# Optimization experiments

Measured on AMD Instinct MI355X. Metric: run time of the kernel, lower is better.

The kernel has to match this reference:

```python
import jax, jax.numpy as jnp
import numpy as np

C = 512
GROUPS = 32
EPS = 1e-6


def group_norm(x, w, b):
    # x: [B, C, H, W]
    B, Cc, H, W = x.shape
    xg = x.reshape(B, GROUPS, Cc // GROUPS, H, W)
    mean = xg.mean(axis=(2, 3, 4), keepdims=True)
    var = xg.var(axis=(2, 3, 4), keepdims=True)
    xn = (xg - mean) * jax.lax.rsqrt(var + EPS)
    xn = xn.reshape(B, Cc, H, W)
    return xn * w[None, :, None, None] + b[None, :, None, None]


def conv1x1(x, w, b):
    # 1x1 conv == per-pixel linear: w [Cout, Cin], x [B, Cin, H, W]
    return jnp.einsum('oc,bchw->bohw', w, x) + b[None, :, None, None]


def setup_inputs() -> dict:
    key = jax.random.key(0)
    ks = jax.random.split(key, 11)
    B, H, W = 4, 64, 64
    s = 1.0 / np.sqrt(C)
    return {
        'x': jax.random.normal(ks[0], (B, C, H, W), dtype=jnp.float32),
        'gn_w': jnp.ones((C,), dtype=jnp.float32),
        'gn_b': jnp.zeros((C,), dtype=jnp.float32),
        'wq': jax.random.normal(ks[1], (C, C), dtype=jnp.float32) * s,
        'bq': jnp.zeros((C,), dtype=jnp.float32),
        'wk': jax.random.normal(ks[2], (C, C), dtype=jnp.float32) * s,
        'bk': jnp.zeros((C,), dtype=jnp.float32),
        'wv': jax.random.normal(ks[3], (C, C), dtype=jnp.float32) * s,
        'bv': jnp.zeros((C,), dtype=jnp.float32),
        'wo': jax.random.normal(ks[4], (C, C), dtype=jnp.float32) * s,
        'bo': jnp.zeros((C,), dtype=jnp.float32),
    }


def reference(x, gn_w, gn_b, wq, bq, wk, bk, wv, bv, wo, bo):
    B, Cc, H, W = x.shape
    scale = Cc ** (-0.5)
    xn = group_norm(x, gn_w, gn_b)
    q = conv1x1(xn, wq, bq).reshape(B, Cc, H * W)
    k = conv1x1(xn, wk, bk).reshape(B, Cc, H * W)
    v = conv1x1(xn, wv, bv).reshape(B, Cc, H * W)
    attn = jax.nn.softmax(jnp.einsum('bci,bcj->bij', q, k) * scale, axis=2)
    out = jnp.einsum('bij,bcj->bci', attn, v).reshape(B, Cc, H, W)
    out = conv1x1(out, wo, bo)
    return x + out
```

## Files before the change

kernel.cpp:

```cpp
#include <hip/hip_runtime.h>

#define NB 4
#define CC 512
#define NSP 4096
#define NGRP 32

using bf16x8 = __attribute__((ext_vector_type(8))) __bf16;
using f32x4  = __attribute__((ext_vector_type(4))) float;

__device__ __forceinline__ unsigned short f2bf(float f) {
  union { float f; unsigned int u; } v; v.f = f;
  unsigned int r = v.u + 0x7fffu + ((v.u >> 16) & 1u);
  return (unsigned short)(r >> 16);
}
__device__ __forceinline__ float bf2f(unsigned short h) {
  union { unsigned int u; float f; } v; v.u = ((unsigned int)h) << 16;
  return v.f;
}

__global__ __launch_bounds__(256) void cvt_w_kernel(const float* __restrict__ wq,
    const float* __restrict__ wk, const float* __restrict__ wv,
    const float* __restrict__ wo, const float* __restrict__ bq,
    const float* __restrict__ bk, unsigned short* __restrict__ wqk,
    unsigned short* __restrict__ wv_bf, unsigned short* __restrict__ wo_bf,
    float* __restrict__ bias_qk, float scale) {
  int i = blockIdx.x * 256 + threadIdx.x;
  wqk[i]          = f2bf(wq[i] * scale);
  wqk[i + 262144] = f2bf(wk[i]);
  wv_bf[i] = f2bf(wv[i]);
  wo_bf[i] = f2bf(wo[i]);
  if (i < 512)        bias_qk[i] = bq[i] * scale;
  else if (i < 1024)  bias_qk[i] = bk[i - 512];
}

__global__ __launch_bounds__(256) void gn_stats_kernel(const float* __restrict__ x,
                                                       float* __restrict__ stats) {
  const int b = blockIdx.x >> 5, g = blockIdx.x & 31;
  const float4* p = reinterpret_cast<const float4*>(x + ((size_t)b * CC + g * 16) * NSP);
  float s = 0.f, ss = 0.f;
  for (int i = threadIdx.x; i < 16384; i += 256) {
    float4 v = p[i];
    s  += v.x + v.y + v.z + v.w;
    ss += v.x * v.x + v.y * v.y + v.z * v.z + v.w * v.w;
  }
  __shared__ float rs[4], rss[4];
  #pragma unroll
  for (int o = 32; o >= 1; o >>= 1) { s += __shfl_down(s, o); ss += __shfl_down(ss, o); }
  if ((threadIdx.x & 63) == 0) { rs[threadIdx.x >> 6] = s; rss[threadIdx.x >> 6] = ss; }
  __syncthreads();
  if (threadIdx.x == 0) {
    s = rs[0] + rs[1] + rs[2] + rs[3];
    ss = rss[0] + rss[1] + rss[2] + rss[3];
    float mean = s * (1.f / 65536.f);
    float var = ss * (1.f / 65536.f) - mean * mean;
    stats[blockIdx.x * 2 + 0] = mean;
    stats[blockIdx.x * 2 + 1] = rsqrtf(var + 1e-6f);
  }
}

__global__ __launch_bounds__(256) void gn_apply_kernel(const float* __restrict__ x,
    const float* __restrict__ stats, const float* __restrict__ gw,
    const float* __restrict__ gb, unsigned short* __restrict__ xnT) {
  const int b = blockIdx.z, c0 = blockIdx.y * 32, n0 = blockIdx.x * 32;
  __shared__ unsigned short tile[32][33];
  const int tx = threadIdx.x & 31, ty = threadIdx.x >> 5;
  #pragma unroll
  for (int r = 0; r < 4; ++r) {
    const int cl = ty + r * 8;
    const int c = c0 + cl;
    const int g = c >> 4;
    const float mean = stats[(b * 32 + g) * 2];
    const float rstd = stats[(b * 32 + g) * 2 + 1];
    const float sc = rstd * gw[c];
    const float sh = gb[c] - mean * sc;
    const float v = x[((size_t)b * CC + c) * NSP + n0 + tx];
    tile[cl][tx] = f2bf(v * sc + sh);
  }
  __syncthreads();
  #pragma unroll
  for (int r = 0; r < 4; ++r) {
    const int nl = ty + r * 8;
    xnT[((size_t)b * NSP + n0 + nl) * CC + c0 + tx] = tile[tx][nl];
  }
}

__global__ __launch_bounds__(256) void sum_reduce_kernel(const float* __restrict__ part,
                                                         float* __restrict__ invl) {
  const int row = blockIdx.x * 4 + (threadIdx.x >> 6);
  const int lane = threadIdx.x & 63;
  float v = part[((size_t)row << 6) + lane];
  #pragma unroll
  for (int msk = 1; msk <= 32; msk <<= 1) v += __shfl_xor(v, msk);
  if (lane == 0) invl[row] = 1.f / v;
}

template<int BIAS, int OMODE, bool RESID, bool INVL>
__global__ __launch_bounds__(256) void gemm2(
    const unsigned short* __restrict__ A, const unsigned short* __restrict__ B,
    const float* __restrict__ bias, const float* __restrict__ resid,
    void* __restrict__ Cout, void* __restrict__ Cout2,
    const float* __restrict__ invl_in, float* __restrict__ part_out,
    int M, int N, int K, float scale,
    long long sAb, long long sBb, long long sCb, long long sRb) {
  __shared__ __align__(16) unsigned short sA[2][128 * 64];
  __shared__ __align__(16) unsigned short sB[2][128 * 64];
  const int tid = threadIdx.x;
  const int lane = tid & 63;
  const int wid  = tid >> 6;

  const unsigned nwg = gridDim.x * gridDim.y * gridDim.z;
  unsigned lin = blockIdx.x + gridDim.x * (blockIdx.y + gridDim.y * blockIdx.z);
  lin = (lin & 7) * (nwg >> 3) + (lin >> 3);
  const int bn = lin % gridDim.x;
  const unsigned t2 = lin / gridDim.x;
  const int bm = t2 % gridDim.y;
  const int b  = t2 / gridDim.y;

  const unsigned short* Ab = A + (size_t)b * sAb + (size_t)bm * 128 * K;
  const unsigned short* Bb = B + (size_t)b * sBb + (size_t)bn * 128 * K;
  const int wm = wid >> 1, wn = wid & 1;
  const int l15 = lane & 15, h = lane >> 4;

  f32x4 acc[4][4] = {};

  auto stage = [&](int buf, int k0) {
    #pragma unroll
    for (int it = 0; it < 4; ++it) {
      const int o  = (it * 256 + tid) * 16;
      const int r  = o >> 7;
      const int c2 = (o & 127) ^ ((r & 7) << 4);
      __builtin_amdgcn_global_load_lds(
          (const __attribute__((address_space(1))) void*)((const char*)(Ab + (size_t)r * K + k0) + c2),
          (__attribute__((address_space(3))) void*)((char*)sA[buf] + o), 16, 0, 0);
      __builtin_amdgcn_global_load_lds(
          (const __attribute__((address_space(1))) void*)((const char*)(Bb + (size_t)r * K + k0) + c2),
          (__attribute__((address_space(3))) void*)((char*)sB[buf] + o), 16, 0, 0);
    }
  };

  int abase[4], bbase[4];
  #pragma unroll
  for (int i = 0; i < 4; ++i) {
    const int ar = wm * 64 + i * 16 + l15;
    abase[i] = ar * 128 + (((ar & 7) << 4) ^ (h << 4));
    const int br = wn * 64 + i * 16 + l15;
    bbase[i] = br * 128 + (((br & 7) << 4) ^ (h << 4));
  }

  stage(0, 0);
  const int NT = K >> 6;
  #pragma unroll 1
  for (int t = 0; t < NT; ++t) {
    const int cur = t & 1;
    if (t + 1 < NT) {
      stage(cur ^ 1, (t + 1) << 6);
      asm volatile("s_waitcnt vmcnt(8)" ::: "memory");
    } else {
      asm volatile("s_waitcnt vmcnt(0)" ::: "memory");
    }
    __builtin_amdgcn_sched_barrier(0);
    __builtin_amdgcn_s_barrier();
    __builtin_amdgcn_sched_barrier(0);

    const char* cA = (const char*)sA[cur];
    const char* cB = (const char*)sB[cur];
    #pragma unroll
    for (int kk = 0; kk < 2; ++kk) {
      bf16x8 af[4], bfr[4];
      #pragma unroll
      for (int m = 0; m < 4; ++m)
        af[m] = *reinterpret_cast<const bf16x8*>(cA + (abase[m] ^ (kk << 6)));
      #pragma unroll
      for (int n = 0; n < 4; ++n)
        bfr[n] = *reinterpret_cast<const bf16x8*>(cB + (bbase[n] ^ (kk << 6)));
      #pragma unroll
      for (int m = 0; m < 4; ++m)
        #pragma unroll
        for (int n = 0; n < 4; ++n)
          acc[m][n] = __builtin_amdgcn_mfma_f32_16x16x32_bf16(af[m], bfr[n], acc[m][n], 0, 0, 0);
    }
    __builtin_amdgcn_sched_barrier(0);
    __builtin_amdgcn_s_barrier();
    __builtin_amdgcn_sched_barrier(0);
  }

  const size_t cb = (size_t)b * sCb;

  if constexpr (OMODE == 2) {
    unsigned short* outh = (unsigned short*)Cout;
    #pragma unroll
    for (int m = 0; m < 4; ++m) {
      #pragma unroll
      for (int r = 0; r < 4; ++r) {
        const int row = bm * 128 + wm * 64 + m * 16 + h * 4 + r;
        float se = 0.f;
        #pragma unroll
        for (int n = 0; n < 4; ++n) {
          const int col = bn * 128 + wn * 64 + n * 16 + l15;
          unsigned short pb = f2bf(__expf(fminf(acc[m][n][r] * scale, 80.f)));
          outh[cb + (size_t)row * N + col] = pb;
          se += bf2f(pb);
        }
        #pragma unroll
        for (int msk = 1; msk <= 8; msk <<= 1) se += __shfl_xor(se, msk);
        if (l15 == 0)
          part_out[(((size_t)b * NSP + row) << 6) + bn * 2 + wn] = se;
      }
    }
    return;
  }

  #pragma unroll
  for (int m = 0; m < 4; ++m) {
    #pragma unroll
    for (int r = 0; r < 4; ++r) {
      const int row = bm * 128 + wm * 64 + m * 16 + h * 4 + r;
      float il = 1.0f;
      if constexpr (INVL) il = invl_in[(size_t)b * NSP + row];
      #pragma unroll
      for (int n = 0; n < 4; ++n) {
        const int col = bn * 128 + wn * 64 + n * 16 + l15;
        float vv = acc[m][n][r];
        if constexpr (BIAS == 1) vv += bias[row];
        if constexpr (BIAS == 2) vv += bias[col];
        vv *= scale;
        if constexpr (INVL) vv *= il;
        if constexpr (RESID) vv += resid[(size_t)b * sRb + (size_t)row * N + col];
        if constexpr (OMODE == 0) {
          ((float*)Cout)[cb + (size_t)row * N + col] = vv;
        } else if constexpr (OMODE == 1) {
          ((unsigned short*)Cout)[cb + (size_t)row * N + col] = f2bf(vv);
        } else {
          unsigned short* dst = (col < 512) ? (unsigned short*)Cout : (unsigned short*)Cout2;
          dst[cb + (size_t)row * 512 + (col & 511)] = f2bf(vv);
        }
      }
    }
  }
}

extern "C" void kernel_launch(void* const* d_in, const int* in_sizes, int n_in,
                              void* d_out, int out_size, void* d_ws, size_t ws_size,
                              hipStream_t stream) {
  const float* x    = (const float*)d_in[0];
  const float* gn_w = (const float*)d_in[1];
  const float* gn_b = (const float*)d_in[2];
  const float* wq   = (const float*)d_in[3];
  const float* bq   = (const float*)d_in[4];
  const float* wk   = (const float*)d_in[5];
  const float* bk   = (const float*)d_in[6];
  const float* wv   = (const float*)d_in[7];
  const float* bv   = (const float*)d_in[8];
  const float* wo   = (const float*)d_in[9];
  const float* bo   = (const float*)d_in[10];
  float* out = (float*)d_out;

  char* ws = (char*)d_ws;
  const size_t NC = (size_t)NSP * CC;
  unsigned short* wqk_bf = (unsigned short*)ws;
  unsigned short* wv_bf  = wqk_bf + 524288;
  unsigned short* wo_bf  = wv_bf + 262144;
  float* bias_qk = (float*)(wo_bf + 262144);
  float* gstats  = bias_qk + 1024;
  unsigned short* xnT = (unsigned short*)(gstats + 512);
  unsigned short* qT  = xnT + NB * NC;
  unsigned short* kT  = qT + NB * NC;
  unsigned short* vC  = kT + NB * NC;
  unsigned short* aoutT = vC + NB * NC;
  unsigned short* S = aoutT + NB * NC;
  float* part = (float*)(S + (size_t)NB * NSP * NSP);
  float* invl = part + ((size_t)NB * NSP << 6);

  const float scale = 0.04419417382415922f;
  const long long SS = (long long)NSP * NSP;

  cvt_w_kernel<<<1024, 256, 0, stream>>>(wq, wk, wv, wo, bq, bk,
                                         wqk_bf, wv_bf, wo_bf, bias_qk, scale);
  gn_stats_kernel<<<NB * NGRP, 256, 0, stream>>>(x, gstats);
  gn_apply_kernel<<<dim3(NSP / 32, CC / 32, NB), 256, 0, stream>>>(x, gstats, gn_w, gn_b, xnT);

  gemm2<2, 3, false, false><<<dim3(1024 / 128, NSP / 128, NB), 256, 0, stream>>>(
      xnT, wqk_bf, bias_qk, nullptr, qT, kT, nullptr, nullptr,
      NSP, 1024, CC, 1.0f, NC, 0, NC, 0);
  gemm2<1, 1, false, false><<<dim3(NSP / 128, CC / 128, NB), 256, 0, stream>>>(
      wv_bf, xnT, bv, nullptr, vC, nullptr, nullptr, nullptr,
      CC, NSP, CC, 1.0f, 0, NC, NC, 0);

  gemm2<0, 2, false, false><<<dim3(NSP / 128, NSP / 128, NB), 256, 0, stream>>>(
      qT, kT, nullptr, nullptr, S, nullptr, nullptr, part,
      NSP, NSP, CC, 1.0f, NC, NC, SS, 0);
  sum_reduce_kernel<<<NB * NSP / 4, 256, 0, stream>>>(part, invl);
  gemm2<0, 1, false, true><<<dim3(CC / 128, NSP / 128, NB), 256, 0, stream>>>(
      S, vC, nullptr, nullptr, aoutT, nullptr, invl, nullptr,
      NSP, CC, NSP, 1.0f, SS, NC, NC, 0);

  gemm2<1, 0, true, false><<<dim3(NSP / 128, CC / 128, NB), 256, 0, stream>>>(
      wo_bf, aoutT, bo, x, out, nullptr, nullptr, nullptr,
      CC, NSP, CC, 1.0f, 0, NC, NC, NC);
}
```

Baseline: 292.2 us.

## Add 512-thread 256-row GEMM with interleaved prefetch for attention matmuls

Adds a new gemm8p kernel that uses 8 waves per block and 256-row tiles (256x256 for QK^T, 256x128 for PV). It interleaves global-to-LDS prefetch of later K-tiles with MFMA phases, using explicit vmcnt waits and setprio. The softmax-exp epilogue and the 1/l normalisation epilogue move into this kernel, and the dead branches are removed from gemm2. The aim is more data reuse per tile and better overlap of loads with compute for the two large attention GEMMs. The cost is more LDS and register pressure, which may lower occupancy.

```diff
diff --git a/kernel.cpp b/kernel.cpp
--- a/kernel.cpp
+++ b/kernel.cpp
@@ -94,12 +94,11 @@
   if (lane == 0) invl[row] = 1.f / v;
 }
 
-template<int BIAS, int OMODE, bool RESID, bool INVL>
+template<int BIAS, int OMODE, bool RESID>
 __global__ __launch_bounds__(256) void gemm2(
     const unsigned short* __restrict__ A, const unsigned short* __restrict__ B,
     const float* __restrict__ bias, const float* __restrict__ resid,
     void* __restrict__ Cout, void* __restrict__ Cout2,
-    const float* __restrict__ invl_in, float* __restrict__ part_out,
     int M, int N, int K, float scale,
     long long sAb, long long sBb, long long sCb, long long sRb) {
   __shared__ __align__(16) unsigned short sA[2][128 * 64];
@@ -185,38 +184,11 @@
   }
 
   const size_t cb = (size_t)b * sCb;
-
-  if constexpr (OMODE == 2) {
-    unsigned short* outh = (unsigned short*)Cout;
-    #pragma unroll
-    for (int m = 0; m < 4; ++m) {
-      #pragma unroll
-      for (int r = 0; r < 4; ++r) {
-        const int row = bm * 128 + wm * 64 + m * 16 + h * 4 + r;
-        float se = 0.f;
-        #pragma unroll
-        for (int n = 0; n < 4; ++n) {
-          const int col = bn * 128 + wn * 64 + n * 16 + l15;
-          unsigned short pb = f2bf(__expf(fminf(acc[m][n][r] * scale, 80.f)));
-          outh[cb + (size_t)row * N + col] = pb;
-          se += bf2f(pb);
-        }
-        #pragma unroll
-        for (int msk = 1; msk <= 8; msk <<= 1) se += __shfl_xor(se, msk);
-        if (l15 == 0)
-          part_out[(((size_t)b * NSP + row) << 6) + bn * 2 + wn] = se;
-      }
-    }
-    return;
-  }
-
   #pragma unroll
   for (int m = 0; m < 4; ++m) {
     #pragma unroll
     for (int r = 0; r < 4; ++r) {
       const int row = bm * 128 + wm * 64 + m * 16 + h * 4 + r;
-      float il = 1.0f;
-      if constexpr (INVL) il = invl_in[(size_t)b * NSP + row];
       #pragma unroll
       for (int n = 0; n < 4; ++n) {
         const int col = bn * 128 + wn * 64 + n * 16 + l15;
@@ -224,7 +196,6 @@
         if constexpr (BIAS == 1) vv += bias[row];
         if constexpr (BIAS == 2) vv += bias[col];
         vv *= scale;
-        if constexpr (INVL) vv *= il;
         if constexpr (RESID) vv += resid[(size_t)b * sRb + (size_t)row * N + col];
         if constexpr (OMODE == 0) {
           ((float*)Cout)[cb + (size_t)row * N + col] = vv;
@@ -233,6 +204,203 @@
         } else {
           unsigned short* dst = (col < 512) ? (unsigned short*)Cout : (unsigned short*)Cout2;
           dst[cb + (size_t)row * 512 + (col & 511)] = f2bf(vv);
+        }
+      }
+    }
+  }
+}
+
+template<int BN, int WMs, int OMODE>
+__global__ __launch_bounds__(512) void gemm8p(
+    const unsigned short* __restrict__ A, const unsigned short* __restrict__ B,
+    void* __restrict__ Cout, const float* __restrict__ invl_in,
+    float* __restrict__ part_out, int N, int K, int lda, int ldb,
+    long long sAb, long long sBb, long long sCb) {
+  constexpr int WNs = 8 / WMs;
+  constexpr int WR = 256 / WMs;
+  constexpr int M_REP = WR / 16;
+  constexpr int BH = BN / 128;
+  __shared__ __align__(16) unsigned short sA[2][256 * 64];
+  __shared__ __align__(16) unsigned short sB[2][BN * 64];
+  const int tid = threadIdx.x;
+  const int lane = tid & 63;
+  const int wid  = tid >> 6;
+
+  const unsigned nwg = gridDim.x * gridDim.y * gridDim.z;
+  unsigned lin = blockIdx.x + gridDim.x * (blockIdx.y + gridDim.y * blockIdx.z);
+  lin = (lin & 7) * (nwg >> 3) + (lin >> 3);
+  const int bn = lin % gridDim.x;
+  const unsigned t2 = lin / gridDim.x;
+  const int bm = t2 % gridDim.y;
+  const int b  = t2 / gridDim.y;
+
+  const unsigned short* Ab = A + (size_t)b * sAb + (size_t)bm * 256 * lda;
+  const unsigned short* Bb = B + (size_t)b * sBb + (size_t)bn * BN * ldb;
+  const int wm = wid / WNs, wn = wid % WNs;
+  const int l15 = lane & 15, h = lane >> 4;
+
+  auto stage_half = [&](const unsigned short* gbase, int ld, int k0, unsigned short* lbase) {
+    #pragma unroll
+    for (int it = 0; it < 2; ++it) {
+      const int o = (it * 512 + tid) * 16;
+      const int r = o >> 7;
+      const int c2 = (o & 127) ^ ((r & 7) << 4);
+      __builtin_amdgcn_global_load_lds(
+          (const __attribute__((address_space(1))) void*)((const char*)(gbase + (size_t)r * ld + k0) + c2),
+          (__attribute__((address_space(3))) void*)((char*)lbase + o), 16, 0, 0);
+    }
+  };
+  auto stageA = [&](int buf, int kt) {
+    stage_half(Ab, lda, kt << 6, &sA[buf][0]);
+  };
+  (void)stageA;
+
+  int abase[M_REP], bbase[4];
+  #pragma unroll
+  for (int i = 0; i < M_REP; ++i) {
+    const int ar = wm * WR + i * 16 + l15;
+    abase[i] = ar * 128 + (((ar & 7) << 4) ^ (h << 4));
+  }
+  #pragma unroll
+  for (int i = 0; i < 4; ++i) {
+    const int br = wn * 64 + i * 16 + l15;
+    bbase[i] = br * 128 + (((br & 7) << 4) ^ (h << 4));
+  }
+
+  f32x4 acc[M_REP][4] = {};
+  const int NT = K >> 6;
+
+  stage_half(Ab, lda, 0, &sA[0][0]);
+  stage_half(Ab + (size_t)128 * lda, lda, 0, &sA[0][128 * 64]);
+  #pragma unroll
+  for (int hs = 0; hs < BH; ++hs)
+    stage_half(Bb + (size_t)hs * 128 * ldb, ldb, 0, &sB[0][hs * 128 * 64]);
+  #pragma unroll
+  for (int hs = 0; hs < BH; ++hs)
+    stage_half(Bb + (size_t)hs * 128 * ldb, ldb, 64, &sB[1][hs * 128 * 64]);
+  if constexpr (BH == 2) asm volatile("s_waitcnt vmcnt(4)" ::: "memory");
+  else                   asm volatile("s_waitcnt vmcnt(2)" ::: "memory");
+  __builtin_amdgcn_sched_barrier(0);
+  __builtin_amdgcn_s_barrier();
+  __builtin_amdgcn_sched_barrier(0);
+
+  #pragma unroll 1
+  for (int u = 0; u < NT; u += 2) {
+    const bool lastit = (u + 2 >= NT);
+    #pragma unroll
+    for (int half = 0; half < 2; ++half) {
+      const char* cA = (const char*)sA[half];
+      const char* cB = (const char*)sB[half];
+      bf16x8 bfr[2][4];
+      #pragma unroll
+      for (int p = 0; p < M_REP / 2; ++p) {
+        if (p == 0) {
+          #pragma unroll
+          for (int kk = 0; kk < 2; ++kk)
+            #pragma unroll
+            for (int n = 0; n < 4; ++n)
+              bfr[kk][n] = *reinterpret_cast<const bf16x8*>(cB + (bbase[n] ^ (kk << 6)));
+        }
+        bf16x8 af[2][2];
+        #pragma unroll
+        for (int i = 0; i < 2; ++i)
+          #pragma unroll
+          for (int kk = 0; kk < 2; ++kk)
+            af[kk][i] = *reinterpret_cast<const bf16x8*>(cA + (abase[2 * p + i] ^ (kk << 6)));
+
+        const int ph = half * (M_REP / 2) + p;
+        if constexpr (M_REP == 8) {
+          if (ph == 0)      stage_half(Ab, lda, (u + 1) << 6, &sA[1][0]);
+          else if (ph == 1) stage_half(Ab + (size_t)128 * lda, lda, (u + 1) << 6, &sA[1][128 * 64]);
+          else if (ph == 2) { if (u + 2 < NT) stage_half(Bb, ldb, (u + 2) << 6, &sB[0][0]); }
+          else if (ph == 3) { if (u + 2 < NT) stage_half(Bb + (size_t)128 * ldb, ldb, (u + 2) << 6, &sB[0][128 * 64]); }
+          else if (ph == 4) { if (u + 2 < NT) stage_half(Ab, lda, (u + 2) << 6, &sA[0][0]); }
+          else if (ph == 5) { if (u + 2 < NT) stage_half(Ab + (size_t)128 * lda, lda, (u + 2) << 6, &sA[0][128 * 64]); }
+          else if (ph == 6) { if (u + 3 < NT) stage_half(Bb, ldb, (u + 3) << 6, &sB[1][0]); }
+          else              { if (u + 3 < NT) stage_half(Bb + (size_t)128 * ldb, ldb, (u + 3) << 6, &sB[1][128 * 64]); }
+        } else {
+          if (ph == 0) {
+            stage_half(Ab, lda, (u + 1) << 6, &sA[1][0]);
+            stage_half(Ab + (size_t)128 * lda, lda, (u + 1) << 6, &sA[1][128 * 64]);
+          } else if (ph == 1) {
+            if (u + 2 < NT) stage_half(Bb, ldb, (u + 2) << 6, &sB[0][0]);
+          } else if (ph == 2) {
+            if (u + 2 < NT) {
+              stage_half(Ab, lda, (u + 2) << 6, &sA[0][0]);
+              stage_half(Ab + (size_t)128 * lda, lda, (u + 2) << 6, &sA[0][128 * 64]);
+            }
+          } else {
+            if (u + 3 < NT) stage_half(Bb, ldb, (u + 3) << 6, &sB[1][0]);
+          }
+        }
+
+        __builtin_amdgcn_sched_barrier(0);
+        __builtin_amdgcn_s_barrier();
+        __builtin_amdgcn_sched_barrier(0);
+        asm volatile("s_waitcnt lgkmcnt(0)" ::: "memory");
+        __builtin_amdgcn_sched_barrier(0);
+        __builtin_amdgcn_s_setprio(1);
+        #pragma unroll
+        for (int i = 0; i < 2; ++i)
+          #pragma unroll
+          for (int n = 0; n < 4; ++n)
+            #pragma unroll
+            for (int kk = 0; kk < 2; ++kk)
+              acc[2 * p + i][n] = __builtin_amdgcn_mfma_f32_16x16x32_bf16(
+                  af[kk][i], bfr[kk][n], acc[2 * p + i][n], 0, 0, 0);
+        __builtin_amdgcn_s_setprio(0);
+        __builtin_amdgcn_sched_barrier(0);
+        if (p == M_REP / 2 - 1) {
+          if (half == 0) {
+            if (lastit) asm volatile("s_waitcnt vmcnt(0)" ::: "memory");
+            else if constexpr (BH == 2) asm volatile("s_waitcnt vmcnt(4)" ::: "memory");
+            else                        asm volatile("s_waitcnt vmcnt(2)" ::: "memory");
+          } else if (!lastit) {
+            if constexpr (BH == 2) asm volatile("s_waitcnt vmcnt(4)" ::: "memory");
+            else                   asm volatile("s_waitcnt vmcnt(2)" ::: "memory");
+          }
+          __builtin_amdgcn_sched_barrier(0);
+        }
+        __builtin_amdgcn_s_barrier();
+        __builtin_amdgcn_sched_barrier(0);
+      }
+    }
+  }
+
+  const size_t cb = (size_t)b * sCb;
+  if constexpr (OMODE == 2) {
+    unsigned short* outh = (unsigned short*)Cout;
+    #pragma unroll
+    for (int m = 0; m < M_REP; ++m) {
+      #pragma unroll
+      for (int r = 0; r < 4; ++r) {
+        const int row = bm * 256 + wm * WR + m * 16 + h * 4 + r;
+        float se = 0.f;
+        #pragma unroll
+        for (int n = 0; n < 4; ++n) {
+          const int col = bn * BN + wn * 64 + n * 16 + l15;
+          unsigned short pb = f2bf(__expf(fminf(acc[m][n][r], 80.f)));
+          outh[cb + (size_t)row * N + col] = pb;
+          se += bf2f(pb);
+        }
+        #pragma unroll
+        for (int msk = 1; msk <= 8; msk <<= 1) se += __shfl_xor(se, msk);
+        if (l15 == 0)
+          part_out[(((size_t)b * NSP + row) << 6) + bn * (BN / 64) + wn] = se;
+      }
+    }
+  } else {
+    unsigned short* outh = (unsigned short*)Cout;
+    #pragma unroll
+    for (int m = 0; m < M_REP; ++m) {
+      #pragma unroll
+      for (int r = 0; r < 4; ++r) {
+        const int row = bm * 256 + wm * WR + m * 16 + h * 4 + r;
+        const float il = invl_in[(size_t)b * NSP + row];
+        #pragma unroll
+        for (int n = 0; n < 4; ++n) {
+          const int col = bn * BN + wn * 64 + n * 16 + l15;
+          outh[cb + (size_t)row * N + col] = f2bf(acc[m][n][r] * il);
         }
       }
     }
@@ -279,22 +447,17 @@
   gn_stats_kernel<<<NB * NGRP, 256, 0, stream>>>(x, gstats);
   gn_apply_kernel<<<dim3(NSP / 32, CC / 32, NB), 256, 0, stream>>>(x, gstats, gn_w, gn_b, xnT);
 
-  gemm2<2, 3, false, false><<<dim3(1024 / 128, NSP / 128, NB), 256, 0, stream>>>(
-      xnT, wqk_bf, bias_qk, nullptr, qT, kT, nullptr, nullptr,
-      NSP, 1024, CC, 1.0f, NC, 0, NC, 0);
-  gemm2<1, 1, false, false><<<dim3(NSP / 128, CC / 128, NB), 256, 0, stream>>>(
-      wv_bf, xnT, bv, nullptr, vC, nullptr, nullptr, nullptr,
-      CC, NSP, CC, 1.0f, 0, NC, NC, 0);
-
-  gemm2<0, 2, false, false><<<dim3(NSP / 128, NSP / 128, NB), 256, 0, stream>>>(
-      qT, kT, nullptr, nullptr, S, nullptr, nullptr, part,
-      NSP, NSP, CC, 1.0f, NC, NC, SS, 0);
+  gemm2<2, 3, false><<<dim3(1024 / 128, NSP / 128, NB), 256, 0, stream>>>(
+      xnT, wqk_bf, bias_qk, nullptr, qT, kT, NSP, 1024, CC, 1.0f, NC, 0, NC, 0);
+  gemm2<1, 1, false><<<dim3(NSP / 128, CC / 128, NB), 256, 0, stream>>>(
+      wv_bf, xnT, bv, nullptr, vC, nullptr, CC, NSP, CC, 1.0f, 0, NC, NC, 0);
+
+  gemm8p<256, 2, 2><<<dim3(NSP / 256, NSP / 256, NB), 512, 0, stream>>>(
+      qT, kT, S, nullptr, part, NSP, CC, CC, CC, NC, NC, SS);
   sum_reduce_kernel<<<NB * NSP / 4, 256, 0, stream>>>(part, invl);
-  gemm2<0, 1, false, true><<<dim3(CC / 128, NSP / 128, NB), 256, 0, stream>>>(
-      S, vC, nullptr, nullptr, aoutT, nullptr, invl, nullptr,
-      NSP, CC, NSP, 1.0f, SS, NC, NC, 0);
-
-  gemm2<1, 0, true, false><<<dim3(NSP / 128, CC / 128, NB), 256, 0, stream>>>(
-      wo_bf, aoutT, bo, x, out, nullptr, nullptr, nullptr,
-      CC, NSP, CC, 1.0f, 0, NC, NC, NC);
-}
+  gemm8p<128, 4, 1><<<dim3(CC / 128, NSP / 256, NB), 512, 0, stream>>>(
+      S, vC, aoutT, invl, nullptr, CC, NSP, NSP, NSP, SS, NC, NC);
+
+  gemm2<1, 0, true><<<dim3(NSP / 128, CC / 128, NB), 256, 0, stream>>>(
+      wo_bf, aoutT, bo, x, out, nullptr, CC, NSP, CC, 1.0f, 0, NC, NC, NC);
+}
```

Measured after the change: 280.3 us. -4.1%, faster.
